# Kernel tuning notes

Hardware: AMD Instinct MI355X
Metric: run time of the kernel (lower is better)

The kernel has to match this reference:

```python
import jax, jax.numpy as jnp
import numpy as np

LMAX = 3                               # self.lmax = lmax_arg(2) + 1
L2 = LMAX * LMAX                       # 9 = 1 + 3 + 5
N_MLP = 2
DEG_IDX = np.repeat(np.arange(LMAX), 2 * np.arange(LMAX) + 1)   # [9] block -> degree index
SEG = np.zeros((LMAX, L2), np.float32)                          # one-hot segment matrix [3,9]
SEG[DEG_IDX, np.arange(L2)] = 1.0


def setup_inputs() -> dict:
    key = jax.random.key(0)
    ks = jax.random.split(key, 8)
    B, M, F, K = 8, 1024, 64, 64
    x = jax.random.normal(ks[0], (B, M, F, L2), jnp.float32)
    y = jax.random.normal(ks[1], (B, M, F, L2), jnp.float32)
    # Glorot-ish scales so tanh stays in its active range
    s0 = 1.0 / np.sqrt(F * F * LMAX)
    sh = 1.0 / np.sqrt(K)
    wx0 = jax.random.normal(ks[2], (K, F, F, LMAX), jnp.float32) * s0
    wy0 = jax.random.normal(ks[3], (K, F, F, LMAX), jnp.float32) * s0
    wx_h = jax.random.normal(ks[4], (N_MLP, K, K), jnp.float32) * sh
    wy_h = jax.random.normal(ks[5], (N_MLP, K, K), jnp.float32) * sh
    wxf = jax.random.normal(ks[6], (LMAX, F, K), jnp.float32) * sh
    wyf = jax.random.normal(ks[7], (LMAX, F, K), jnp.float32) * sh
    return {"x": x, "y": y, "wx0": wx0, "wy0": wy0,
            "wx_h": wx_h, "wy_h": wy_h, "wxf": wxf, "wyf": wyf}


def reference(x, y, wx0, wy0, wx_h, wy_h, wxf, wyf):
    seg = jnp.asarray(SEG)                                   # [lmax, l2]
    # cross-product gate from the l=1 (vector) components
    x1 = x[..., 1:4]                                         # [B,M,F,3]
    y1 = y[..., 1:4]
    gate = jnp.sum(jnp.cross(x1, y1) * y[..., 0:3], axis=-1) # [B,M,F]
    xg = x * gate[..., None]                                 # gated x, [B,M,F,l2]
    # outer product over features + contiguous segment-sum over degree blocks
    # mix[b,m,f,g,l] = sum_{s in block l} xg[b,m,g,s] * y[b,m,f,s]
    mix = jnp.einsum('bmgs,bmfs,ls->bmfgl', xg, y, seg)      # [B,M,F,F,lmax]
    mix_x = jnp.einsum('bmfgl,kfgl->bmk', mix, wx0)          # [B,M,k]
    mix_y = jnp.einsum('bmfgl,kfgl->bmk', mix, wy0)
    for i in range(N_MLP):
        mix_x = jnp.tanh(mix_x @ wx_h[i])
        mix_y = jnp.tanh(mix_y @ wy_h[i])
    mix_x = jnp.tanh(jnp.einsum('bmk,lfk->bmfl', mix_x, wxf))  # [B,M,F,lmax]
    mix_y = jnp.tanh(jnp.einsum('bmk,lfk->bmfl', mix_y, wyf))
    # broadcast each degree back over its 2l+1 components (gather == tf.repeat)
    res = mix_x[..., DEG_IDX] * xg + mix_y[..., DEG_IDX] * y   # [B,M,F,l2]
    return res
```

## Files before the change

kernel.cpp:

```cpp
#include <hip/hip_runtime.h>
#include <hip/hip_bf16.h>

typedef __attribute__((ext_vector_type(8))) short short8;
typedef __attribute__((ext_vector_type(16))) float f32x16;
typedef __fp16 h2 __attribute__((ext_vector_type(2)));
typedef unsigned short ushort_t;

#define DEVFN static __device__ __forceinline__
#define MFMA32 __builtin_amdgcn_mfma_f32_32x32x16_bf16

DEVFN float bf2f(unsigned short u){
  union { unsigned int i; float f; } v; v.i = ((unsigned int)u) << 16; return v.f;
}
DEVFN unsigned short f2bf(float f){
  unsigned int u = __float_as_uint(f);
  unsigned int r = u + 0x7FFFu + ((u >> 16) & 1u);
  return (unsigned short)(r >> 16);
}
DEVFN unsigned int pkbf(float a, float b){
  unsigned int r;
  asm("v_cvt_pk_bf16_f32 %0, %1, %2" : "=v"(r) : "v"(a), "v"(b));
  return r;
}
DEVFN h2 pkrtz(float a, float b){ return __builtin_amdgcn_cvt_pkrtz(a, b); }
DEVFN h2 u2h(unsigned int u){ union { unsigned int u; h2 h; } v; v.u = u; return v.h; }
#if __has_builtin(__builtin_amdgcn_fdot2)
DEVFN float fdot2(h2 a, h2 b, float c){ return __builtin_amdgcn_fdot2(a, b, c, false); }
#else
DEVFN float fdot2(h2 a, h2 b, float c){ return c + (float)a[0]*(float)b[0] + (float)a[1]*(float)b[1]; }
#endif
DEVFN float tanh_fast(float x){
  float t = __builtin_amdgcn_exp2f(x * 2.885390081777926815f);
  return 1.0f - 2.0f * __builtin_amdgcn_rcpf(t + 1.0f);
}
DEVFN int kmap(int h, int j){ return 4*h + (j & 3) + 8*(j >> 2); }

__global__ void bake_w0(const float* __restrict__ wx0, const float* __restrict__ wy0,
                        ushort_t* __restrict__ wfrag){
  int idx = blockIdx.x * 256 + threadIdx.x;
  int g = idx & 63; int r = idx >> 6;
  int f = r & 63; r >>= 6;
  int k = r & 63; int path = r >> 6;
  const float* w = path ? wy0 : wx0;
  const float* src = w + ((size_t)(k*64 + f)*64 + g)*3;
  float v0 = src[0], v1 = src[1], v2 = src[2];
  int gq = g >> 4, gl = g & 15;
  int h = (gl >> 2) & 1;
  int j = (gl & 3) | ((gl >> 3) << 2);
  int lane = h*32 + (k & 31);
  int nt = k >> 5;
  size_t base = (size_t)((f*4 + gq)*2 + path)*3072 + (size_t)lane*8 + j;
  wfrag[base + 0*512 + (size_t)nt*512] = f2bf(v0);
  wfrag[base + 2*512 + (size_t)nt*512] = f2bf(v1);
  wfrag[base + 4*512 + (size_t)nt*512] = f2bf(v2);
}

__global__ void bake_wh(const float* __restrict__ wxh, const float* __restrict__ wyh,
                        ushort_t* __restrict__ whfrag){
  int slot = blockIdx.x * 256 + threadIdx.x;
  int lane = slot & 63;
  int q = slot >> 6;
  int nt = q & 1; q >>= 1;
  int c  = q & 3; q >>= 2;
  int path = q & 1; int layer = q >> 1;
  const float* w = path ? wyh : wxh;
  int n = nt*32 + (lane & 31);
  int h = lane >> 5;
  unsigned int pk[4];
#pragma unroll
  for (int jj = 0; jj < 4; ++jj){
    int k0 = c*16 + kmap(h, 2*jj);
    int k1 = c*16 + kmap(h, 2*jj + 1);
    unsigned int b0 = f2bf(w[layer*4096 + k0*64 + n]);
    unsigned int b1 = f2bf(w[layer*4096 + k1*64 + n]);
    pk[jj] = b0 | (b1 << 16);
  }
  *reinterpret_cast<uint4*>(whfrag + (size_t)slot * 8) = make_uint4(pk[0], pk[1], pk[2], pk[3]);
}

__global__ void bake_wf(const float* __restrict__ wxf, const float* __restrict__ wyf,
                        ushort_t* __restrict__ wffrag){
  int slot = blockIdx.x * 256 + threadIdx.x;
  int lane = slot & 63;
  int q = slot >> 6;
  int ntf = q % 6;
  int q2 = q / 6;
  int c = q2 & 3; int path = q2 >> 2;
  const float* w = path ? wyf : wxf;
  int n = ntf*32 + (lane & 31);
  int lw = n >> 6, fw = n & 63;
  int h = lane >> 5;
  unsigned int pk[4];
#pragma unroll
  for (int jj = 0; jj < 4; ++jj){
    int k0 = c*16 + kmap(h, 2*jj);
    int k1 = c*16 + kmap(h, 2*jj + 1);
    unsigned int b0 = f2bf(w[(lw*64 + fw)*64 + k0]);
    unsigned int b1 = f2bf(w[(lw*64 + fw)*64 + k1]);
    pk[jj] = b0 | (b1 << 16);
  }
  *reinterpret_cast<uint4*>(wffrag + (size_t)slot * 8) = make_uint4(pk[0], pk[1], pk[2], pk[3]);
}

struct BSet { uint4 b[6]; };
union U4 { uint4 u; short8 s; };

__global__ __launch_bounds__(256)
void gemm10(const float* __restrict__ x, const float* __restrict__ y,
            const ushort_t* __restrict__ wfrag, float* __restrict__ mix){
  extern __shared__ char lds[];
  unsigned int* YHd = (unsigned int*)lds;
  ushort_t* YHh = (ushort_t*)lds;
  float (*red)[33] = (float (*)[33])(lds + 41600);

  const int bid = blockIdx.x;
  const int id = (bid & 7)*64 + (bid >> 3);
  const int nh = id & 1, mb = id >> 1;
  const int pbase = mb * 32;

  const int t = threadIdx.x, lane = t & 63, gq = t >> 6;
  const int h = lane >> 5, pr = lane & 31;

  const float* yb = y + (size_t)pbase * 576;

#pragma unroll
  for (int c = 0; c < 18; ++c){
    int q = t + c*256;
    int p = q / 144, off = (q - p*144) * 4;
    float4 v = *(const float4*)(yb + p*576 + off);
#pragma unroll
    for (int i = 0; i < 4; ++i){
      int flat = off + i;
      int f = flat / 9, s = flat - f*9;
      float vv = (i==0) ? v.x : (i==1) ? v.y : (i==2) ? v.z : v.w;
      union { __fp16 hf; ushort_t u; } cv; cv.hf = (__fp16)vv;
      YHh[p*650 + f*10 + s] = cv.u;
    }
  }
  __syncthreads();

  h2 xg[8][5];
#pragma unroll
  for (int j = 0; j < 8; ++j){
    const int g = gq*16 + kmap(h, j);
    const float* xp = x + (size_t)(pbase + pr)*576 + g*9;
    unsigned int yd0 = YHd[pr*325 + g*5 + 0];
    unsigned int yd1 = YHd[pr*325 + g*5 + 1];
    h2 y01 = u2h(yd0), y23v = u2h(yd1);
    float y0 = (float)y01[0], y1 = (float)y01[1];
    float y2 = (float)y23v[0], y3 = (float)y23v[1];
    float x1 = xp[1], x2 = xp[2], x3 = xp[3];
    float gate = (x2*y3 - x3*y2)*y0 + (x3*y1 - x1*y3)*y1 + (x1*y2 - x2*y1)*y2;
    xg[j][0] = pkrtz(xp[0]*gate, x1*gate);
    xg[j][1] = pkrtz(x2*gate, x3*gate);
    xg[j][2] = pkrtz(xp[4]*gate, xp[5]*gate);
    xg[j][3] = pkrtz(xp[6]*gate, xp[7]*gate);
    xg[j][4] = pkrtz(xp[8]*gate, 0.f);
  }

  f32x16 acc0, acc1;
#pragma unroll
  for (int e = 0; e < 16; ++e){ acc0[e] = 0.f; acc1[e] = 0.f; }

  const ushort_t* wt = wfrag + (size_t)(gq*2 + nh)*3072 + (size_t)lane*8;
  const unsigned int* yrow = YHd + pr*325;

  auto ldB = [&](int f, BSet& B){
    const ushort_t* p0 = wt + (size_t)f * 24576;
#pragma unroll
    for (int i = 0; i < 6; ++i) B.b[i] = *reinterpret_cast<const uint4*>(p0 + i*512);
  };
  auto ldYh = [&](int f, unsigned int* Yr){
#pragma unroll
    for (int d = 0; d < 5; ++d) Yr[d] = yrow[f*5 + d];
  };
  auto agen_mfma = [&](const unsigned int* Yr, const BSet& B){
    h2 y0m = u2h(Yr[0] & 0xFFFFu);
    h2 y1m = u2h(Yr[0] & 0xFFFF0000u);
    h2 y23 = u2h(Yr[1]), y45 = u2h(Yr[2]), y67 = u2h(Yr[3]);
    h2 y8p = u2h(Yr[4] & 0xFFFFu);
    float a0[8], a1[8], a2[8];
#pragma unroll
    for (int j = 0; j < 8; ++j){
      a0[j] = fdot2(xg[j][0], y0m, 0.f);
      a1[j] = fdot2(xg[j][1], y23, fdot2(xg[j][0], y1m, 0.f));
      a2[j] = fdot2(xg[j][4], y8p, fdot2(xg[j][3], y67, fdot2(xg[j][2], y45, 0.f)));
    }
    U4 fA0, fA1, fA2;
    fA0.u = make_uint4(pkbf(a0[0],a0[1]), pkbf(a0[2],a0[3]), pkbf(a0[4],a0[5]), pkbf(a0[6],a0[7]));
    fA1.u = make_uint4(pkbf(a1[0],a1[1]), pkbf(a1[2],a1[3]), pkbf(a1[4],a1[5]), pkbf(a1[6],a1[7]));
    fA2.u = make_uint4(pkbf(a2[0],a2[1]), pkbf(a2[2],a2[3]), pkbf(a2[4],a2[5]), pkbf(a2[6],a2[7]));
    U4 b0, b1, b2, b3, b4, b5;
    b0.u = B.b[0]; b1.u = B.b[1]; b2.u = B.b[2];
    b3.u = B.b[3]; b4.u = B.b[4]; b5.u = B.b[5];
    acc0 = MFMA32(fA0.s, b0.s, acc0, 0, 0, 0);
    acc1 = MFMA32(fA0.s, b1.s, acc1, 0, 0, 0);
    acc0 = MFMA32(fA1.s, b2.s, acc0, 0, 0, 0);
    acc1 = MFMA32(fA1.s, b3.s, acc1, 0, 0, 0);
    acc0 = MFMA32(fA2.s, b4.s, acc0, 0, 0, 0);
    acc1 = MFMA32(fA2.s, b5.s, acc1, 0, 0, 0);
  };

  BSet Ba, Bb;
  unsigned int Ya[5], Yb[5];
  ldB(0, Ba); ldYh(0, Ya);
  ldB(1, Bb); ldYh(1, Yb);

#pragma unroll 1
  for (int s = 0; s < 64; s += 2){
    agen_mfma(Ya, Ba);
    const int s2 = (s + 2 < 64) ? s + 2 : 63;
    ldB(s2, Ba); ldYh(s2, Ya);
    agen_mfma(Yb, Bb);
    const int s3 = (s + 3 < 64) ? s + 3 : 63;
    ldB(s3, Bb); ldYh(s3, Yb);
  }

  __syncthreads();
#pragma unroll 1
  for (int rr = 1; rr <= 3; ++rr){
    if (gq == rr){
#pragma unroll
      for (int e = 0; e < 16; ++e){
        red[lane][e]      = acc0[e];
        red[lane][16 + e] = acc1[e];
      }
    }
    __syncthreads();
    if (gq == 0){
#pragma unroll
      for (int e = 0; e < 16; ++e){
        acc0[e] += red[lane][e];
        acc1[e] += red[lane][16 + e];
      }
    }
    __syncthreads();
  }
  if (gq == 0){
#pragma unroll
    for (int e = 0; e < 16; ++e){
      int rowm = (e & 3) + 8*(e >> 2) + 4*h;
      float* d = mix + (size_t)(pbase + rowm)*128 + nh*64 + pr;
      d[0]  = acc0[e];
      d[32] = acc1[e];
    }
  }
}

__global__ __launch_bounds__(256, 1)
void mlp_final(const float* __restrict__ x, const float* __restrict__ y,
               const ushort_t* __restrict__ whfrag,
               const ushort_t* __restrict__ wffrag,
               const float* __restrict__ mix, float* __restrict__ out){
  extern __shared__ char ldsm[];
  ushort_t* hw = (ushort_t*)ldsm;
  const int t = threadIdx.x;
  const long pbase = (long)blockIdx.x * 32;

  {
    int p = t >> 3, n0 = (t & 7) * 16;
    const float* src = mix + (pbase + p)*128 + n0;
    int path = n0 >> 6, nn = n0 & 63;
    ushort_t* dst = hw + (path*2)*2176 + p*68 + nn;
#pragma unroll
    for (int q2 = 0; q2 < 16; ++q2) dst[q2] = f2bf(src[q2]);
  }
  __syncthreads();

  const int w = t >> 6, lane = t & 63;
  const int path = w >> 1, ntw = w & 1;
  const int prow = lane & 31, h = lane >> 5;
  int cur = 0;

#pragma unroll
  for (int layer = 0; layer < 2; ++layer){
    const ushort_t* act = hw + (path*2 + cur)*2176;
    f32x16 acc;
#pragma unroll
    for (int r = 0; r < 16; ++r) acc[r] = 0.f;
#pragma unroll
    for (int c = 0; c < 4; ++c){
      int ab = prow*68 + c*16 + 4*h;
      ushort4 lo = *(const ushort4*)&act[ab];
      ushort4 hi = *(const ushort4*)&act[ab + 8];
      short8 av; av[0]=lo.x; av[1]=lo.y; av[2]=lo.z; av[3]=lo.w;
      av[4]=hi.x; av[5]=hi.y; av[6]=hi.z; av[7]=hi.w;
      short8 bv = *(const short8*)(whfrag + ((((layer*2 + path)*4 + c)*2 + ntw)*512 + lane*8));
      acc = MFMA32(av, bv, acc, 0, 0, 0);
    }
    ushort_t* nact = hw + (path*2 + (cur ^ 1))*2176;
#pragma unroll
    for (int r = 0; r < 16; ++r){
      int p = (r & 3) + 8*(r >> 2) + 4*h;
      nact[p*68 + ntw*32 + prow] = f2bf(tanh_fast(acc[r]));
    }
    cur ^= 1;
    __syncthreads();
  }

  {
    const ushort_t* act = hw + (path*2 + cur)*2176;
    ushort_t* ob = hw + 8704 + path*6272;
#pragma unroll
    for (int e = 0; e < 3; ++e){
      int ntf = ntw*3 + e;
      f32x16 acc;
#pragma unroll
      for (int r = 0; r < 16; ++r) acc[r] = 0.f;
#pragma unroll
      for (int c = 0; c < 4; ++c){
        int ab = prow*68 + c*16 + 4*h;
        ushort4 lo = *(const ushort4*)&act[ab];
        ushort4 hi = *(const ushort4*)&act[ab + 8];
        short8 av; av[0]=lo.x; av[1]=lo.y; av[2]=lo.z; av[3]=lo.w;
        av[4]=hi.x; av[5]=hi.y; av[6]=hi.z; av[7]=hi.w;
        short8 bv = *(const short8*)(wffrag + (((path*4 + c)*6 + ntf)*512 + lane*8));
        acc = MFMA32(av, bv, acc, 0, 0, 0);
      }
#pragma unroll
      for (int r = 0; r < 16; ++r){
        int p = (r & 3) + 8*(r >> 2) + 4*h;
        ob[p*196 + ntf*32 + prow] = f2bf(tanh_fast(acc[r]));
      }
    }
  }
  __syncthreads();

  const ushort_t* oxb = hw + 8704;
  const ushort_t* oyb = hw + 8704 + 6272;
#pragma unroll 1
  for (int rep = 0; rep < 8; ++rep){
    int idx = t + rep*256;
    int p = idx >> 6, fq = idx & 63;
    const float* xr = x + ((pbase + p)*64 + fq)*9;
    const float* yr = y + ((pbase + p)*64 + fq)*9;
    float xv[9], yv[9];
#pragma unroll
    for (int s = 0; s < 9; ++s){ xv[s] = xr[s]; yv[s] = yr[s]; }
    float c0 = xv[2]*yv[3] - xv[3]*yv[2];
    float c1 = xv[3]*yv[1] - xv[1]*yv[3];
    float c2 = xv[1]*yv[2] - xv[2]*yv[1];
    float gate = c0*yv[0] + c1*yv[1] + c2*yv[2];
    float ox0 = bf2f(oxb[p*196 + fq]);
    float ox1 = bf2f(oxb[p*196 + 64 + fq]);
    float ox2 = bf2f(oxb[p*196 + 128 + fq]);
    float oy0 = bf2f(oyb[p*196 + fq]);
    float oy1 = bf2f(oyb[p*196 + 64 + fq]);
    float oy2 = bf2f(oyb[p*196 + 128 + fq]);
    float* orow = out + ((pbase + p)*64 + fq)*9;
    orow[0] = ox0*xv[0]*gate + oy0*yv[0];
#pragma unroll
    for (int s = 1; s < 4; ++s) orow[s] = ox1*xv[s]*gate + oy1*yv[s];
#pragma unroll
    for (int s = 4; s < 9; ++s) orow[s] = ox2*xv[s]*gate + oy2*yv[s];
  }
}

extern "C" void kernel_launch(void* const* d_in, const int* in_sizes, int n_in,
                              void* d_out, int out_size, void* d_ws, size_t ws_size,
                              hipStream_t stream){
  (void)in_sizes; (void)n_in; (void)out_size; (void)ws_size;
  const float* x   = (const float*)d_in[0];
  const float* y   = (const float*)d_in[1];
  const float* wx0 = (const float*)d_in[2];
  const float* wy0 = (const float*)d_in[3];
  const float* wxh = (const float*)d_in[4];
  const float* wyh = (const float*)d_in[5];
  const float* wxf = (const float*)d_in[6];
  const float* wyf = (const float*)d_in[7];
  float* out = (float*)d_out;
  char* ws = (char*)d_ws;
  ushort_t* wfrag  = (ushort_t*)(ws);
  ushort_t* whfrag = (ushort_t*)(ws + 3145728);
  ushort_t* wffrag = (ushort_t*)(ws + 3178496);
  float* mix       = (float*)(ws + 3227648);

  (void)hipFuncSetAttribute((const void*)gemm10,
        hipFuncAttributeMaxDynamicSharedMemorySize, 50048);
  (void)hipFuncSetAttribute((const void*)mlp_final,
        hipFuncAttributeMaxDynamicSharedMemorySize, 43520);

  hipLaunchKernelGGL(bake_w0, dim3(2048), dim3(256), 0, stream, wx0, wy0, wfrag);
  hipLaunchKernelGGL(bake_wh, dim3(8),    dim3(256), 0, stream, wxh, wyh, whfrag);
  hipLaunchKernelGGL(bake_wf, dim3(12),   dim3(256), 0, stream, wxf, wyf, wffrag);
  hipLaunchKernelGGL(gemm10,  dim3(512),  dim3(256), 50048, stream, x, y, wfrag, mix);
  hipLaunchKernelGGL(mlp_final, dim3(256), dim3(256), 42496, stream, x, y, whfrag, wffrag, mix, out);
}
```

Measured before the change: 90.78 us.

## Split gemm reduction over f into two halves with partial-sum buffers

Splits the main mixing GEMM's f-dimension in two, launching twice as many blocks that each handle 32 of the 64 f values. Each block writes its result to a separate partial buffer, and mlp_final sums the two partials when it loads them. The y tile held in LDS shrinks, so the gate now reads y straight from global memory. MFMA issue priority is raised with s_setprio. The change targets low occupancy and the long serial loop, at the cost of extra partial-buffer traffic and more reduction work.

```diff
diff --git a/kernel.cpp b/kernel.cpp
--- a/kernel.cpp
+++ b/kernel.cpp
@@ -106,16 +106,16 @@
 union U4 { uint4 u; short8 s; };
 
 __global__ __launch_bounds__(256)
-void gemm10(const float* __restrict__ x, const float* __restrict__ y,
-            const ushort_t* __restrict__ wfrag, float* __restrict__ mix){
+void gemm11(const float* __restrict__ x, const float* __restrict__ y,
+            const ushort_t* __restrict__ wfrag, float* __restrict__ mixp){
   extern __shared__ char lds[];
   unsigned int* YHd = (unsigned int*)lds;
   ushort_t* YHh = (ushort_t*)lds;
-  float (*red)[33] = (float (*)[33])(lds + 41600);
+  float (*red)[33] = (float (*)[33])(lds + 21120);
 
   const int bid = blockIdx.x;
-  const int id = (bid & 7)*64 + (bid >> 3);
-  const int nh = id & 1, mb = id >> 1;
+  const int id = (bid & 7)*128 + (bid >> 3);
+  const int fh = id & 1, nh = (id >> 1) & 1, mb = id >> 2;
   const int pbase = mb * 32;
 
   const int t = threadIdx.x, lane = t & 63, gq = t >> 6;
@@ -124,17 +124,17 @@
   const float* yb = y + (size_t)pbase * 576;
 
 #pragma unroll
-  for (int c = 0; c < 18; ++c){
+  for (int c = 0; c < 9; ++c){
     int q = t + c*256;
-    int p = q / 144, off = (q - p*144) * 4;
-    float4 v = *(const float4*)(yb + p*576 + off);
+    int p = q / 72, off = (q - p*72) * 4;
+    float4 v = *(const float4*)(yb + p*576 + fh*288 + off);
 #pragma unroll
     for (int i = 0; i < 4; ++i){
       int flat = off + i;
       int f = flat / 9, s = flat - f*9;
       float vv = (i==0) ? v.x : (i==1) ? v.y : (i==2) ? v.z : v.w;
       union { __fp16 hf; ushort_t u; } cv; cv.hf = (__fp16)vv;
-      YHh[p*650 + f*10 + s] = cv.u;
+      YHh[p*330 + f*10 + s] = cv.u;
     }
   }
   __syncthreads();
@@ -144,11 +144,8 @@
   for (int j = 0; j < 8; ++j){
     const int g = gq*16 + kmap(h, j);
     const float* xp = x + (size_t)(pbase + pr)*576 + g*9;
-    unsigned int yd0 = YHd[pr*325 + g*5 + 0];
-    unsigned int yd1 = YHd[pr*325 + g*5 + 1];
-    h2 y01 = u2h(yd0), y23v = u2h(yd1);
-    float y0 = (float)y01[0], y1 = (float)y01[1];
-    float y2 = (float)y23v[0], y3 = (float)y23v[1];
+    const float* yp = y + (size_t)(pbase + pr)*576 + g*9;
+    float y0 = yp[0], y1 = yp[1], y2 = yp[2], y3 = yp[3];
     float x1 = xp[1], x2 = xp[2], x3 = xp[3];
     float gate = (x2*y3 - x3*y2)*y0 + (x3*y1 - x1*y3)*y1 + (x1*y2 - x2*y1)*y2;
     xg[j][0] = pkrtz(xp[0]*gate, x1*gate);
@@ -162,11 +159,11 @@
 #pragma unroll
   for (int e = 0; e < 16; ++e){ acc0[e] = 0.f; acc1[e] = 0.f; }
 
-  const ushort_t* wt = wfrag + (size_t)(gq*2 + nh)*3072 + (size_t)lane*8;
-  const unsigned int* yrow = YHd + pr*325;
-
-  auto ldB = [&](int f, BSet& B){
-    const ushort_t* p0 = wt + (size_t)f * 24576;
+  const ushort_t* wt = wfrag + (size_t)(fh*32)*24576
+                             + (size_t)(gq*2 + nh)*3072 + (size_t)lane*8;
+  const unsigned int* yrow = YHd + pr*165;
+
+  auto ldB = [&](const ushort_t* p0, BSet& B){
 #pragma unroll
     for (int i = 0; i < 6; ++i) B.b[i] = *reinterpret_cast<const uint4*>(p0 + i*512);
   };
@@ -193,28 +190,32 @@
     U4 b0, b1, b2, b3, b4, b5;
     b0.u = B.b[0]; b1.u = B.b[1]; b2.u = B.b[2];
     b3.u = B.b[3]; b4.u = B.b[4]; b5.u = B.b[5];
+    __builtin_amdgcn_s_setprio(1);
     acc0 = MFMA32(fA0.s, b0.s, acc0, 0, 0, 0);
     acc1 = MFMA32(fA0.s, b1.s, acc1, 0, 0, 0);
     acc0 = MFMA32(fA1.s, b2.s, acc0, 0, 0, 0);
     acc1 = MFMA32(fA1.s, b3.s, acc1, 0, 0, 0);
     acc0 = MFMA32(fA2.s, b4.s, acc0, 0, 0, 0);
     acc1 = MFMA32(fA2.s, b5.s, acc1, 0, 0, 0);
+    __builtin_amdgcn_s_setprio(0);
   };
 
   BSet Ba, Bb;
   unsigned int Ya[5], Yb[5];
-  ldB(0, Ba); ldYh(0, Ya);
-  ldB(1, Bb); ldYh(1, Yb);
+  const ushort_t* wpa = wt;
+  const ushort_t* wpb = wt + 24576;
+  ldB(wpa, Ba); ldYh(0, Ya);
+  ldB(wpb, Bb); ldYh(1, Yb);
 
 #pragma unroll 1
-  for (int s = 0; s < 64; s += 2){
+  for (int s = 0; s < 30; s += 2){
     agen_mfma(Ya, Ba);
-    const int s2 = (s + 2 < 64) ? s + 2 : 63;
-    ldB(s2, Ba); ldYh(s2, Ya);
+    wpa += 49152; ldB(wpa, Ba); ldYh(s + 2, Ya);
     agen_mfma(Yb, Bb);
-    const int s3 = (s + 3 < 64) ? s + 3 : 63;
-    ldB(s3, Bb); ldYh(s3, Yb);
-  }
+    wpb += 49152; ldB(wpb, Bb); ldYh(s + 3, Yb);
+  }
+  agen_mfma(Ya, Ba);
+  agen_mfma(Yb, Bb);
 
   __syncthreads();
 #pragma unroll 1
@@ -237,10 +238,11 @@
     __syncthreads();
   }
   if (gq == 0){
+    float* mp = mixp + (size_t)fh * 1048576;
 #pragma unroll
     for (int e = 0; e < 16; ++e){
       int rowm = (e & 3) + 8*(e >> 2) + 4*h;
-      float* d = mix + (size_t)(pbase + rowm)*128 + nh*64 + pr;
+      float* d = mp + (size_t)(pbase + rowm)*128 + nh*64 + pr;
       d[0]  = acc0[e];
       d[32] = acc1[e];
     }
@@ -251,7 +253,7 @@
 void mlp_final(const float* __restrict__ x, const float* __restrict__ y,
                const ushort_t* __restrict__ whfrag,
                const ushort_t* __restrict__ wffrag,
-               const float* __restrict__ mix, float* __restrict__ out){
+               const float* __restrict__ mixp, float* __restrict__ out){
   extern __shared__ char ldsm[];
   ushort_t* hw = (ushort_t*)ldsm;
   const int t = threadIdx.x;
@@ -259,11 +261,14 @@
 
   {
     int p = t >> 3, n0 = (t & 7) * 16;
-    const float* src = mix + (pbase + p)*128 + n0;
+    const float* src = mixp + (pbase + p)*128 + n0;
     int path = n0 >> 6, nn = n0 & 63;
     ushort_t* dst = hw + (path*2)*2176 + p*68 + nn;
 #pragma unroll
-    for (int q2 = 0; q2 < 16; ++q2) dst[q2] = f2bf(src[q2]);
+    for (int q2 = 0; q2 < 16; ++q2){
+      float v = src[q2] + src[q2 + 1048576];
+      dst[q2] = f2bf(v);
+    }
   }
   __syncthreads();
 
@@ -373,16 +378,16 @@
   ushort_t* wfrag  = (ushort_t*)(ws);
   ushort_t* whfrag = (ushort_t*)(ws + 3145728);
   ushort_t* wffrag = (ushort_t*)(ws + 3178496);
-  float* mix       = (float*)(ws + 3227648);
-
-  (void)hipFuncSetAttribute((const void*)gemm10,
-        hipFuncAttributeMaxDynamicSharedMemorySize, 50048);
+  float* mixp      = (float*)(ws + 3227648);
+
+  (void)hipFuncSetAttribute((const void*)gemm11,
+        hipFuncAttributeMaxDynamicSharedMemorySize, 29568);
   (void)hipFuncSetAttribute((const void*)mlp_final,
         hipFuncAttributeMaxDynamicSharedMemorySize, 43520);
 
   hipLaunchKernelGGL(bake_w0, dim3(2048), dim3(256), 0, stream, wx0, wy0, wfrag);
   hipLaunchKernelGGL(bake_wh, dim3(8),    dim3(256), 0, stream, wxh, wyh, whfrag);
   hipLaunchKernelGGL(bake_wf, dim3(12),   dim3(256), 0, stream, wxf, wyf, wffrag);
-  hipLaunchKernelGGL(gemm10,  dim3(512),  dim3(256), 50048, stream, x, y, wfrag, mix);
-  hipLaunchKernelGGL(mlp_final, dim3(256), dim3(256), 42496, stream, x, y, whfrag, wffrag, mix, out);
-}
+  hipLaunchKernelGGL(gemm11,  dim3(1024), dim3(256), 29568, stream, x, y, wfrag, mixp);
+  hipLaunchKernelGGL(mlp_final, dim3(256), dim3(256), 42496, stream, x, y, whfrag, wffrag, mixp, out);
+}
```

Result: slower. 94.18 us (+3.8%).

## Split MLP and epilogue into separate kernels with coalesced LDS-staged epilogue

Applied to the files above, without the earlier changes.

The fused mlp_final kernel ran on only 256 blocks, one per CU, with a strided per-thread epilogue reading 9 floats each. It is split into mlp_core, which writes the bf16 final activations to a global workspace, and a new epilogue_k launched on 2048 blocks. epilogue_k stages x and y through LDS with float4 loads and writes the output back coalesced. This adds a kernel launch and a global round trip of the small bf16 activation buffers, in exchange for more parallelism and better memory coalescing in the bandwidth-heavy epilogue.

```diff
diff --git a/kernel.cpp b/kernel.cpp
--- a/kernel.cpp
+++ b/kernel.cpp
@@ -248,10 +248,10 @@
 }
 
 __global__ __launch_bounds__(256, 1)
-void mlp_final(const float* __restrict__ x, const float* __restrict__ y,
-               const ushort_t* __restrict__ whfrag,
-               const ushort_t* __restrict__ wffrag,
-               const float* __restrict__ mix, float* __restrict__ out){
+void mlp_core(const ushort_t* __restrict__ whfrag,
+              const ushort_t* __restrict__ wffrag,
+              const float* __restrict__ mix,
+              ushort_t* __restrict__ oxg, ushort_t* __restrict__ oyg){
   extern __shared__ char ldsm[];
   ushort_t* hw = (ushort_t*)ldsm;
   const int t = threadIdx.x;
@@ -300,7 +300,7 @@
 
   {
     const ushort_t* act = hw + (path*2 + cur)*2176;
-    ushort_t* ob = hw + 8704 + path*6272;
+    ushort_t* og = (path ? oyg : oxg) + (size_t)pbase * 196;
 #pragma unroll
     for (int e = 0; e < 3; ++e){
       int ntf = ntw*3 + e;
@@ -320,20 +320,35 @@
 #pragma unroll
       for (int r = 0; r < 16; ++r){
         int p = (r & 3) + 8*(r >> 2) + 4*h;
-        ob[p*196 + ntf*32 + prow] = f2bf(tanh_fast(acc[r]));
+        og[(size_t)p*196 + ntf*32 + prow] = f2bf(tanh_fast(acc[r]));
       }
     }
   }
+}
+
+__global__ __launch_bounds__(256)
+void epilogue_k(const float* __restrict__ x, const float* __restrict__ y,
+                const ushort_t* __restrict__ oxg, const ushort_t* __restrict__ oyg,
+                float* __restrict__ out){
+  __shared__ float xs[2304], ys[2304], os[2304];
+  const int t = threadIdx.x;
+  const long pbase = (long)blockIdx.x * 4;
+  const float4* xb = (const float4*)(x + pbase*576);
+  const float4* yb = (const float4*)(y + pbase*576);
+#pragma unroll
+  for (int c = 0; c < 3; ++c){
+    int q = t + c*256;
+    if (q < 576){
+      ((float4*)xs)[q] = xb[q];
+      ((float4*)ys)[q] = yb[q];
+    }
+  }
   __syncthreads();
 
-  const ushort_t* oxb = hw + 8704;
-  const ushort_t* oyb = hw + 8704 + 6272;
-#pragma unroll 1
-  for (int rep = 0; rep < 8; ++rep){
-    int idx = t + rep*256;
-    int p = idx >> 6, fq = idx & 63;
-    const float* xr = x + ((pbase + p)*64 + fq)*9;
-    const float* yr = y + ((pbase + p)*64 + fq)*9;
+  const int pp = t >> 6, fq = t & 63;
+  {
+    const float* xr = &xs[pp*576 + fq*9];
+    const float* yr = &ys[pp*576 + fq*9];
     float xv[9], yv[9];
 #pragma unroll
     for (int s = 0; s < 9; ++s){ xv[s] = xr[s]; yv[s] = yr[s]; }
@@ -341,18 +356,27 @@
     float c1 = xv[3]*yv[1] - xv[1]*yv[3];
     float c2 = xv[1]*yv[2] - xv[2]*yv[1];
     float gate = c0*yv[0] + c1*yv[1] + c2*yv[2];
-    float ox0 = bf2f(oxb[p*196 + fq]);
-    float ox1 = bf2f(oxb[p*196 + 64 + fq]);
-    float ox2 = bf2f(oxb[p*196 + 128 + fq]);
-    float oy0 = bf2f(oyb[p*196 + fq]);
-    float oy1 = bf2f(oyb[p*196 + 64 + fq]);
-    float oy2 = bf2f(oyb[p*196 + 128 + fq]);
-    float* orow = out + ((pbase + p)*64 + fq)*9;
+    const size_t prow = (size_t)(pbase + pp) * 196;
+    float ox0 = bf2f(oxg[prow + fq]);
+    float ox1 = bf2f(oxg[prow + 64 + fq]);
+    float ox2 = bf2f(oxg[prow + 128 + fq]);
+    float oy0 = bf2f(oyg[prow + fq]);
+    float oy1 = bf2f(oyg[prow + 64 + fq]);
+    float oy2 = bf2f(oyg[prow + 128 + fq]);
+    float* orow = &os[pp*576 + fq*9];
     orow[0] = ox0*xv[0]*gate + oy0*yv[0];
 #pragma unroll
     for (int s = 1; s < 4; ++s) orow[s] = ox1*xv[s]*gate + oy1*yv[s];
 #pragma unroll
     for (int s = 4; s < 9; ++s) orow[s] = ox2*xv[s]*gate + oy2*yv[s];
+  }
+  __syncthreads();
+
+  float4* ob = (float4*)(out + pbase*576);
+#pragma unroll
+  for (int c = 0; c < 3; ++c){
+    int q = t + c*256;
+    if (q < 576) ob[q] = ((const float4*)os)[q];
   }
 }
 
@@ -374,15 +398,16 @@
   ushort_t* whfrag = (ushort_t*)(ws + 3145728);
   ushort_t* wffrag = (ushort_t*)(ws + 3178496);
   float* mix       = (float*)(ws + 3227648);
+  ushort_t* oxg    = (ushort_t*)(ws + 7421952);
+  ushort_t* oyg    = (ushort_t*)(ws + 10633216);
 
   (void)hipFuncSetAttribute((const void*)gemm10,
         hipFuncAttributeMaxDynamicSharedMemorySize, 50048);
-  (void)hipFuncSetAttribute((const void*)mlp_final,
-        hipFuncAttributeMaxDynamicSharedMemorySize, 43520);
 
   hipLaunchKernelGGL(bake_w0, dim3(2048), dim3(256), 0, stream, wx0, wy0, wfrag);
   hipLaunchKernelGGL(bake_wh, dim3(8),    dim3(256), 0, stream, wxh, wyh, whfrag);
   hipLaunchKernelGGL(bake_wf, dim3(12),   dim3(256), 0, stream, wxf, wyf, wffrag);
   hipLaunchKernelGGL(gemm10,  dim3(512),  dim3(256), 50048, stream, x, y, wfrag, mix);
-  hipLaunchKernelGGL(mlp_final, dim3(256), dim3(256), 42496, stream, x, y, whfrag, wffrag, mix, out);
-}
+  hipLaunchKernelGGL(mlp_core, dim3(256), dim3(256), 17408, stream, whfrag, wffrag, mix, oxg, oyg);
+  hipLaunchKernelGGL(epilogue_k, dim3(2048), dim3(256), 0, stream, x, y, oxg, oyg, out);
+}
```

After: 86.05 us. 1.05x faster.
